# Performance work log

Hardware: AMD Instinct MI355X
Metric: run time of the kernel (lower is better)

The kernel has to match this reference:

```python
import jax, jax.numpy as jnp
import numpy as np
import math

B, Q, CQ = 2, 2048, 512
H, D = 8, 64  # no_heads, c_hidden

def setup_inputs() -> dict:
    key = jax.random.key(0)
    ks = jax.random.split(key, 8)
    s = 0.02
    return {
        "q_x": jax.random.normal(ks[0], (B, Q, CQ), jnp.float32),
        "kv_x": jax.random.normal(ks[1], (B, Q, CQ), jnp.float32),
        "bias": jax.random.normal(ks[2], (B, 1, Q, Q), jnp.float32),
        "w_qkv": jax.random.normal(ks[3], (3 * H * D, CQ), jnp.float32) * s,
        "w_o": jax.random.normal(ks[4], (CQ, H * D), jnp.float32) * s,
        "b_o": jnp.zeros((CQ,), jnp.float32),
        "w_g": jax.random.normal(ks[5], (H * D, CQ), jnp.float32) * s,
        "b_g": jnp.zeros((H * D,), jnp.float32),
    }

def reference(q_x, kv_x, bias, w_qkv, w_o, b_o, w_g, b_g):
    # Fused QKV projection from q_x (kv_x is unused by the original module's _prep_qkv)
    qkv = jnp.einsum('bqc,ec->bqe', q_x, w_qkv)  # [B,Q,3*H*D]
    q, k, v = jnp.split(qkv, 3, axis=-1)
    q = q.reshape(B, Q, H, D) / math.sqrt(D)
    k = k.reshape(B, Q, H, D)
    v = v.reshape(B, Q, H, D)
    # scores + additive pairwise bias, softmax over keys
    scores = jnp.einsum('bqhd,bkhd->bhqk', q, k) + bias  # [B,H,Q,K]
    attn = jax.nn.softmax(scores, axis=-1)
    o = jnp.einsum('bhqk,bkhd->bqhd', attn, v)  # [B,Q,H,D]
    # sigmoid gating
    g = jax.nn.sigmoid(jnp.einsum('bqc,ec->bqe', q_x, w_g) + b_g).reshape(B, Q, H, D)
    o = o * g
    # output projection
    o = o.reshape(B, Q, H * D)
    return jnp.einsum('bqe,ce->bqc', o, w_o) + b_o
```

## Files before the change

kernel.cpp:

```cpp
#include <hip/hip_runtime.h>
#include <math.h>

#define B_  2
#define Q_  2048
#define CQ_ 512
#define H_  8
#define D_  64
#define M_  (B_*Q_)
#define L2E 1.44269504088896f

typedef __bf16 bf16;
typedef __bf16 bf16x4 __attribute__((ext_vector_type(4)));
typedef __bf16 bf16x8 __attribute__((ext_vector_type(8)));
typedef float  f32x4  __attribute__((ext_vector_type(4)));
typedef float  f32x16 __attribute__((ext_vector_type(16)));

__device__ __forceinline__ void gl_lds16(const bf16* g, bf16* l) {
    __builtin_amdgcn_global_load_lds(
        (const __attribute__((address_space(1))) unsigned int*)g,
        (__attribute__((address_space(3))) unsigned int*)l, 16, 0, 0);
}

#define S0 (4096*512)
#define S1 (1536*512)
#define S2 (512*512)
#define S3 (512*512)
__global__ __launch_bounds__(256)
void convert_kernel(const float* __restrict__ qx, const float* __restrict__ wqkv,
                    const float* __restrict__ wg, const float* __restrict__ wo,
                    bf16* __restrict__ qxb, bf16* __restrict__ wcat, bf16* __restrict__ wob)
{
    const long long t = (long long)blockIdx.x * 256 + threadIdx.x;
    const long long e = t * 8;
    const float* src; bf16* dst;
    if (e < S0)                { src = qx + e;                  dst = qxb + e; }
    else if (e < S0 + S1)      { src = wqkv + (e - S0);         dst = wcat + (e - S0); }
    else if (e < S0 + S1 + S2) { src = wg + (e - S0 - S1);      dst = wcat + S1 + (e - S0 - S1); }
    else                       { src = wo + (e - S0 - S1 - S2); dst = wob + (e - S0 - S1 - S2); }
    const float4 a = *(const float4*)(src);
    const float4 b = *(const float4*)(src + 4);
    bf16x8 v;
    v[0] = (bf16)a.x; v[1] = (bf16)a.y; v[2] = (bf16)a.z; v[3] = (bf16)a.w;
    v[4] = (bf16)b.x; v[5] = (bf16)b.y; v[6] = (bf16)b.z; v[7] = (bf16)b.w;
    *(bf16x8*)dst = v;
}

template<int BM, int BN, int EPI>
__global__ __launch_bounds__(256)
void gemm_bf16(const bf16* __restrict__ A, const bf16* __restrict__ W,
               const float* __restrict__ bvec, float* __restrict__ fout,
               bf16* __restrict__ qb, bf16* __restrict__ kb, bf16* __restrict__ vb,
               bf16* __restrict__ gb)
{
    constexpr int MI = BM / 32, NJ = BN / 32;
    __shared__ __align__(16) bf16 As[BM * 32];
    __shared__ __align__(16) bf16 Bs[BN * 32];

    const int t = threadIdx.x;
    const int w = t >> 6, lane = t & 63;
    const int l15 = lane & 15, quad = lane >> 4;
    const int wm = w & 1, wn = w >> 1;
    const int bm = blockIdx.x * BM;
    const int bn = blockIdx.y * BN;
    const bool swapped = (EPI == 1) || ((bn >> 9) != 2);

    f32x4 acc[MI][NJ] = {};

    const int rr = t >> 2;
    const int cc = (t & 3) * 8;

    for (int k0 = 0; k0 < 512; k0 += 32) {
        #pragma unroll
        for (int i = 0; i < BM / 64; ++i)
            gl_lds16(A + (size_t)(bm + i * 64 + rr) * 512 + k0 + cc,
                     As + (i * 64 + w * 16) * 32);
        #pragma unroll
        for (int i = 0; i < BN / 64; ++i)
            gl_lds16(W + (size_t)(bn + i * 64 + rr) * 512 + k0 + cc,
                     Bs + (i * 64 + w * 16) * 32);
        __asm__ volatile("s_waitcnt vmcnt(0)" ::: "memory");
        __syncthreads();

        bf16x8 af[MI], bfr[NJ];
        #pragma unroll
        for (int i = 0; i < MI; ++i)
            af[i] = *(const bf16x8*)(As + (wm * (BM / 2) + i * 16 + l15) * 32 + quad * 8);
        #pragma unroll
        for (int j = 0; j < NJ; ++j)
            bfr[j] = *(const bf16x8*)(Bs + (wn * (BN / 2) + j * 16 + l15) * 32 + quad * 8);
        if (swapped) {
            #pragma unroll
            for (int i = 0; i < MI; ++i)
                #pragma unroll
                for (int j = 0; j < NJ; ++j)
                    acc[i][j] = __builtin_amdgcn_mfma_f32_16x16x32_bf16(bfr[j], af[i], acc[i][j], 0, 0, 0);
        } else {
            #pragma unroll
            for (int i = 0; i < MI; ++i)
                #pragma unroll
                for (int j = 0; j < NJ; ++j)
                    acc[i][j] = __builtin_amdgcn_mfma_f32_16x16x32_bf16(af[i], bfr[j], acc[i][j], 0, 0, 0);
        }
        __syncthreads();
    }

    if (swapped) {
        #pragma unroll
        for (int i = 0; i < MI; ++i) {
            const int m = bm + wm * (BM / 2) + i * 16 + l15;
            const int b = m >> 11, qq = m & 2047;
            #pragma unroll
            for (int j = 0; j < NJ; ++j) {
                const int n0 = bn + wn * (BN / 2) + j * 16 + quad * 4;
                const f32x4 cv = acc[i][j];
                if constexpr (EPI == 1) {
                    float4 st;
                    st.x = cv[0] + bvec[n0 + 0];
                    st.y = cv[1] + bvec[n0 + 1];
                    st.z = cv[2] + bvec[n0 + 2];
                    st.w = cv[3] + bvec[n0 + 3];
                    *(float4*)(fout + (size_t)m * 512 + n0) = st;
                } else {
                    const int part = n0 >> 9;
                    if (part == 0) {
                        const int h = (n0 >> 6) & 7, d0 = n0 & 63;
                        bf16x4 q4;
                        #pragma unroll
                        for (int r = 0; r < 4; ++r) q4[r] = (bf16)(cv[r] * (0.125f * L2E));
                        *(bf16x4*)(qb + (size_t)(b * H_ + h) * (Q_ * D_) + (size_t)qq * 64 + d0) = q4;
                    } else if (part == 1) {
                        const int h = (n0 >> 6) & 7, d0 = n0 & 63;
                        const size_t off = (size_t)(b * H_ + h) * (Q_ * D_)
                            + (qq >> 6) * 4096 + ((qq >> 5) & 1) * 2048
                            + (d0 >> 4) * 512 + ((d0 >> 3) & 1) * 256
                            + (qq & 31) * 8 + (d0 & 7);
                        bf16x4 k4;
                        #pragma unroll
                        for (int r = 0; r < 4; ++r) k4[r] = (bf16)cv[r];
                        *(bf16x4*)(kb + off) = k4;
                    } else {
                        const int gcol = n0 & 511;
                        const float4 bv4 = *(const float4*)(bvec + gcol);
                        bf16x4 g4;
                        g4[0] = (bf16)(1.f / (1.f + __expf(-(cv[0] + bv4.x))));
                        g4[1] = (bf16)(1.f / (1.f + __expf(-(cv[1] + bv4.y))));
                        g4[2] = (bf16)(1.f / (1.f + __expf(-(cv[2] + bv4.z))));
                        g4[3] = (bf16)(1.f / (1.f + __expf(-(cv[3] + bv4.w))));
                        *(bf16x4*)(gb + (size_t)m * 512 + gcol) = g4;
                    }
                }
            }
        }
    } else {
        #pragma unroll
        for (int i = 0; i < MI; ++i) {
            const int m0 = bm + wm * (BM / 2) + i * 16 + quad * 4;
            const int b = m0 >> 11, qq0 = m0 & 2047;
            #pragma unroll
            for (int j = 0; j < NJ; ++j) {
                const int n = bn + wn * (BN / 2) + j * 16 + l15;
                const int h = (n >> 6) & 7, d = n & 63;
                const size_t off = (size_t)(b * H_ + h) * (Q_ * D_)
                    + (qq0 >> 6) * 4096 + (d >> 5) * 2048
                    + ((qq0 & 63) >> 4) * 512 + ((qq0 >> 3) & 1) * 256
                    + (d & 31) * 8 + (qq0 & 7);
                bf16x4 v4;
                #pragma unroll
                for (int r = 0; r < 4; ++r) v4[r] = (bf16)acc[i][j][r];
                *(bf16x4*)(vb + off) = v4;
            }
        }
    }
}

__global__ __launch_bounds__(256, 3)
void attn_part(const bf16* __restrict__ qb, const bf16* __restrict__ kf,
               const bf16* __restrict__ vf, const float* __restrict__ bias,
               bf16* __restrict__ po, float* __restrict__ lsum)
{
    __shared__ __align__(16) bf16 Ks[2][4096];
    __shared__ __align__(16) bf16 Vs[2][4096];
    __shared__ __align__(16) bf16 Ps[4][32 * 72];

    const int tid  = threadIdx.x;
    const int wv   = tid >> 6, lane = tid & 63;
    const int l31  = lane & 31, b5 = lane >> 5;
    const int x    = blockIdx.x;
    const int bh   = ((x & 7) << 1) | (x >> 3);
    const int b    = bh >> 3;
    const int qg   = blockIdx.y * 128 + wv * 32 + l31;
    const int ks   = blockIdx.z;
    const int nsteps = (ks < 2) ? 12 : 8;

    const bf16* qp = qb + ((size_t)bh * Q_ + qg) * D_;
    bf16x8 bq[4];
    #pragma unroll
    for (int c = 0; c < 4; ++c)
        bq[c] = *(const bf16x8*)(qp + c * 16 + b5 * 8);

    f32x16 acc[2] = {};
    float l_loc = 0.f;

    const bf16*  kfb  = kf + (size_t)bh * (Q_ * D_) + (size_t)ks * 12 * 4096;
    const bf16*  vfb  = vf + (size_t)bh * (Q_ * D_) + (size_t)ks * 12 * 4096;
    const float* brow = bias + ((size_t)b * Q_ + qg) * Q_ + ks * 768;

    f32x4 bcur[8], bnxt[8];

    #pragma unroll
    for (int p = 0; p < 2; ++p) {
        gl_lds16(kfb + (wv * 2 + p) * 512 + lane * 8, Ks[0] + (wv * 2 + p) * 512);
        gl_lds16(vfb + (wv * 2 + p) * 512 + lane * 8, Vs[0] + (wv * 2 + p) * 512);
    }
    #pragma unroll
    for (int i = 0; i < 8; ++i)
        bcur[i] = *(const f32x4*)(brow + (i >> 2) * 32 + (i & 3) * 8 + b5 * 4);
    __asm__ volatile("s_waitcnt vmcnt(0)" ::: "memory");
    __syncthreads();

    bf16* pw = Ps[wv] + l31 * 72;

    int cur = 0;
    #pragma unroll 1
    for (int t = 0; t < nsteps; ++t) {
        if (t + 1 < nsteps) {
            const size_t off = (size_t)(t + 1) * 4096;
            #pragma unroll
            for (int p = 0; p < 2; ++p) {
                gl_lds16(kfb + off + (wv * 2 + p) * 512 + lane * 8,
                         Ks[cur ^ 1] + (wv * 2 + p) * 512);
                gl_lds16(vfb + off + (wv * 2 + p) * 512 + lane * 8,
                         Vs[cur ^ 1] + (wv * 2 + p) * 512);
            }
            const int k0n = (t + 1) * 64;
            #pragma unroll
            for (int i = 0; i < 8; ++i)
                bnxt[i] = *(const f32x4*)(brow + k0n + (i >> 2) * 32 + (i & 3) * 8 + b5 * 4);
        }

        const bf16* Kc = Ks[cur];
        f32x16 sv[2] = {};
        #pragma unroll
        for (int kg = 0; kg < 2; ++kg)
            #pragma unroll
            for (int c = 0; c < 4; ++c) {
                const bf16x8 ak = *(const bf16x8*)(Kc + kg * 2048 + c * 512 + lane * 8);
                sv[kg] = __builtin_amdgcn_mfma_f32_32x32x16_bf16(ak, bq[c], sv[kg], 0, 0, 0);
            }

        float sc[2][16];
        float rsum = 0.f;
        #pragma unroll
        for (int kg = 0; kg < 2; ++kg)
            #pragma unroll
            for (int r = 0; r < 16; ++r) {
                sc[kg][r] = __builtin_amdgcn_exp2f(
                    fmaf(bcur[kg * 4 + (r >> 2)][r & 3], L2E, sv[kg][r]));
                rsum += sc[kg][r];
            }
        l_loc += rsum;

        #pragma unroll
        for (int kg = 0; kg < 2; ++kg)
            #pragma unroll
            for (int gi = 0; gi < 4; ++gi) {
                bf16x4 p4;
                p4[0] = (bf16)sc[kg][gi * 4 + 0];
                p4[1] = (bf16)sc[kg][gi * 4 + 1];
                p4[2] = (bf16)sc[kg][gi * 4 + 2];
                p4[3] = (bf16)sc[kg][gi * 4 + 3];
                *(bf16x4*)(pw + kg * 32 + gi * 8 + b5 * 4) = p4;
            }
        __asm__ volatile("s_waitcnt lgkmcnt(0)" ::: "memory");

        const bf16* Vc = Vs[cur];
        #pragma unroll
        for (int c4 = 0; c4 < 4; ++c4) {
            const bf16x8 bp = *(const bf16x8*)(pw + c4 * 16 + b5 * 8);
            #pragma unroll
            for (int dg = 0; dg < 2; ++dg) {
                const bf16x8 av = *(const bf16x8*)(Vc + dg * 2048 + c4 * 512 + lane * 8);
                acc[dg] = __builtin_amdgcn_mfma_f32_32x32x16_bf16(av, bp, acc[dg], 0, 0, 0);
            }
        }

        if (t + 1 < nsteps) {
            #pragma unroll
            for (int i = 0; i < 8; ++i) bcur[i] = bnxt[i];
        }
        __asm__ volatile("s_waitcnt vmcnt(0)" ::: "memory");
        __syncthreads();
        cur ^= 1;
    }

    const float l_run = l_loc + __shfl_xor(l_loc, 32, 64);
    const size_t pbase = ((size_t)(ks * 16 + bh) * Q_ + qg) * 64;
    #pragma unroll
    for (int dg = 0; dg < 2; ++dg)
        #pragma unroll
        for (int gi = 0; gi < 4; ++gi) {
            const int d0 = dg * 32 + gi * 8 + b5 * 4;
            bf16x4 ov;
            #pragma unroll
            for (int r = 0; r < 4; ++r)
                ov[r] = (bf16)acc[dg][gi * 4 + r];
            *(bf16x4*)(po + pbase + d0) = ov;
        }
    if (b5 == 0)
        lsum[(size_t)(ks * 16 + bh) * Q_ + qg] = l_run;
}

__global__ __launch_bounds__(256)
void merge_kernel(const bf16* __restrict__ po, const float* __restrict__ lsum,
                  const bf16* g, bf16* og)
{
    const int gid = blockIdx.x * 256 + threadIdx.x;
    const int row = gid >> 3;
    const int d8  = (gid & 7) * 8;
    const int bh  = row >> 11, qg = row & 2047;
    const int b   = bh >> 3, h = bh & 7;

    const float inv = 1.f / (lsum[row] + lsum[16 * Q_ + row] + lsum[32 * Q_ + row]);

    const bf16x8 o0 = *(const bf16x8*)(po + (size_t)row * 64 + d8);
    const bf16x8 o1 = *(const bf16x8*)(po + (size_t)16 * Q_ * 64 + (size_t)row * 64 + d8);
    const bf16x8 o2 = *(const bf16x8*)(po + (size_t)32 * Q_ * 64 + (size_t)row * 64 + d8);
    const size_t obase = ((size_t)(b * Q_ + qg)) * 512 + h * 64 + d8;
    const bf16x8 gv = *(const bf16x8*)(g + obase);
    bf16x8 ov;
    #pragma unroll
    for (int r = 0; r < 8; ++r)
        ov[r] = (bf16)(((float)o0[r] + (float)o1[r] + (float)o2[r]) * inv * (float)gv[r]);
    *(bf16x8*)(og + obase) = ov;
}

extern "C" void kernel_launch(void* const* d_in, const int* in_sizes, int n_in,
                              void* d_out, int out_size, void* d_ws, size_t ws_size,
                              hipStream_t stream)
{
    const float* q_x   = (const float*)d_in[0];
    const float* bias  = (const float*)d_in[2];
    const float* w_qkv = (const float*)d_in[3];
    const float* w_o   = (const float*)d_in[4];
    const float* b_o   = (const float*)d_in[5];
    const float* w_g   = (const float*)d_in[6];
    const float* b_g   = (const float*)d_in[7];
    float* out = (float*)d_out;

    char* ws = (char*)d_ws;
    bf16*  po   = (bf16*)(ws);
    bf16*  qxb  = (bf16*)(ws);
    bf16*  wcat = (bf16*)(ws + (4u  << 20));
    bf16*  qb   = (bf16*)(ws + (12u << 20));
    bf16*  kb   = (bf16*)(ws + (16u << 20));
    bf16*  vb   = (bf16*)(ws + (20u << 20));
    bf16*  gb   = (bf16*)(ws + (24u << 20));
    bf16*  wob  = (bf16*)(ws + (28u << 20));
    float* lsum = (float*)(ws + (28u << 20) + (1u << 19));

    convert_kernel<<<(S0 + S1 + S2 + S3) / (256 * 8), 256, 0, stream>>>(
        q_x, w_qkv, w_g, w_o, qxb, wcat, wob);
    gemm_bf16<128, 64, 0><<<dim3(32, 32), 256, 0, stream>>>(
        qxb, wcat, b_g, nullptr, qb, kb, vb, gb);
    attn_part<<<dim3(B_ * H_, Q_ / 128, 3), 256, 0, stream>>>(qb, kb, vb, bias, po, lsum);
    merge_kernel<<<(16 * Q_ * 8) / 256, 256, 0, stream>>>(po, lsum, gb, gb);
    gemm_bf16<64, 64, 1><<<dim3(64, 8), 256, 0, stream>>>(
        gb, wob, b_o, out, nullptr, nullptr, nullptr, nullptr);
}
```

Before: 189.9 us.

## Pack GEMM operands k-major, double-buffer GEMM LDS, shuffle P in registers

The convert kernel now writes q_x and the weights in a k-panel-major packed layout, so each GEMM stage becomes contiguous 16-byte global-to-LDS copies. The GEMM gains double-buffered LDS so the next k-slice is fetched while MFMAs run on the current one. In attention, the P tile is passed between half-waves with cross-lane shuffles instead of an LDS round trip, the key split across the three z-slices is rebalanced to 11/11/10, and bias is loaded inside each step rather than prefetched a step ahead. The bias change trades prefetch overlap for lower register pressure, and the doubled GEMM LDS may reduce occupancy.

```diff
diff --git a/kernel.cpp b/kernel.cpp
--- a/kernel.cpp
+++ b/kernel.cpp
@@ -19,6 +19,14 @@
     __builtin_amdgcn_global_load_lds(
         (const __attribute__((address_space(1))) unsigned int*)g,
         (__attribute__((address_space(3))) unsigned int*)l, 16, 0, 0);
+}
+
+__device__ __forceinline__ bf16x4 shfl_xor32(bf16x4 v) {
+    union { bf16x4 h; int i[2]; } u;
+    u.h = v;
+    u.i[0] = __shfl_xor(u.i[0], 32, 64);
+    u.i[1] = __shfl_xor(u.i[1], 32, 64);
+    return u.h;
 }
 
 #define S0 (4096*512)
@@ -33,10 +41,26 @@
     const long long t = (long long)blockIdx.x * 256 + threadIdx.x;
     const long long e = t * 8;
     const float* src; bf16* dst;
-    if (e < S0)                { src = qx + e;                  dst = qxb + e; }
-    else if (e < S0 + S1)      { src = wqkv + (e - S0);         dst = wcat + (e - S0); }
-    else if (e < S0 + S1 + S2) { src = wg + (e - S0 - S1);      dst = wcat + S1 + (e - S0 - S1); }
-    else                       { src = wo + (e - S0 - S1 - S2); dst = wob + (e - S0 - S1 - S2); }
+    if (e < S0) {
+        const int m = (int)(e >> 9), k = (int)(e & 511);
+        src = qx + e;
+        dst = qxb + (size_t)(k >> 5) * (4096 * 32) + (size_t)m * 32 + (k & 31);
+    } else if (e < S0 + S1) {
+        const long long e2 = e - S0;
+        const int n = (int)(e2 >> 9), k = (int)(e2 & 511);
+        src = wqkv + e2;
+        dst = wcat + (size_t)(k >> 5) * (2048 * 32) + (size_t)n * 32 + (k & 31);
+    } else if (e < S0 + S1 + S2) {
+        const long long e2 = e - S0 - S1;
+        const int n = 1536 + (int)(e2 >> 9), k = (int)(e2 & 511);
+        src = wg + e2;
+        dst = wcat + (size_t)(k >> 5) * (2048 * 32) + (size_t)n * 32 + (k & 31);
+    } else {
+        const long long e2 = e - S0 - S1 - S2;
+        const int n = (int)(e2 >> 9), k = (int)(e2 & 511);
+        src = wo + e2;
+        dst = wob + (size_t)(k >> 5) * (512 * 32) + (size_t)n * 32 + (k & 31);
+    }
     const float4 a = *(const float4*)(src);
     const float4 b = *(const float4*)(src + 4);
     bf16x8 v;
@@ -45,7 +69,7 @@
     *(bf16x8*)dst = v;
 }
 
-template<int BM, int BN, int EPI>
+template<int BM, int BN, int EPI, int WNR, int APACK>
 __global__ __launch_bounds__(256)
 void gemm_bf16(const bf16* __restrict__ A, const bf16* __restrict__ W,
                const float* __restrict__ bvec, float* __restrict__ fout,
@@ -53,8 +77,9 @@
                bf16* __restrict__ gb)
 {
     constexpr int MI = BM / 32, NJ = BN / 32;
-    __shared__ __align__(16) bf16 As[BM * 32];
-    __shared__ __align__(16) bf16 Bs[BN * 32];
+    constexpr int APARTS = BM / 16, BPARTS = BN / 16, NPARTS = APARTS + BPARTS;
+    __shared__ __align__(16) bf16 As[2][BM * 32];
+    __shared__ __align__(16) bf16 Bs[2][BN * 32];
 
     const int t = threadIdx.x;
     const int w = t >> 6, lane = t & 63;
@@ -66,28 +91,40 @@
 
     f32x4 acc[MI][NJ] = {};
 
-    const int rr = t >> 2;
-    const int cc = (t & 3) * 8;
-
-    for (int k0 = 0; k0 < 512; k0 += 32) {
-        #pragma unroll
-        for (int i = 0; i < BM / 64; ++i)
-            gl_lds16(A + (size_t)(bm + i * 64 + rr) * 512 + k0 + cc,
-                     As + (i * 64 + w * 16) * 32);
-        #pragma unroll
-        for (int i = 0; i < BN / 64; ++i)
-            gl_lds16(W + (size_t)(bn + i * 64 + rr) * 512 + k0 + cc,
-                     Bs + (i * 64 + w * 16) * 32);
-        __asm__ volatile("s_waitcnt vmcnt(0)" ::: "memory");
-        __syncthreads();
+    auto stage = [&](int kp, int buf) {
+        #pragma unroll
+        for (int idx = 0; idx < NPARTS / 4; ++idx) {
+            const int p = idx * 4 + w;
+            if (p < APARTS) {
+                if constexpr (APACK)
+                    gl_lds16(A + (size_t)kp * (4096 * 32) + (size_t)bm * 32 + p * 512 + lane * 8,
+                             As[buf] + p * 512);
+                else
+                    gl_lds16(A + (size_t)(bm + p * 16 + (lane >> 2)) * 512 + kp * 32 + (lane & 3) * 8,
+                             As[buf] + p * 512);
+            } else {
+                gl_lds16(W + (size_t)kp * (WNR * 32) + (size_t)bn * 32 + (p - APARTS) * 512 + lane * 8,
+                         Bs[buf] + (p - APARTS) * 512);
+            }
+        }
+    };
+
+    stage(0, 0);
+    __asm__ volatile("s_waitcnt vmcnt(0)" ::: "memory");
+    __syncthreads();
+
+    int cur = 0;
+    #pragma unroll 1
+    for (int kp = 0; kp < 16; ++kp) {
+        if (kp < 15) stage(kp + 1, cur ^ 1);
 
         bf16x8 af[MI], bfr[NJ];
         #pragma unroll
         for (int i = 0; i < MI; ++i)
-            af[i] = *(const bf16x8*)(As + (wm * (BM / 2) + i * 16 + l15) * 32 + quad * 8);
+            af[i] = *(const bf16x8*)(As[cur] + (wm * (BM / 2) + i * 16 + l15) * 32 + quad * 8);
         #pragma unroll
         for (int j = 0; j < NJ; ++j)
-            bfr[j] = *(const bf16x8*)(Bs + (wn * (BN / 2) + j * 16 + l15) * 32 + quad * 8);
+            bfr[j] = *(const bf16x8*)(Bs[cur] + (wn * (BN / 2) + j * 16 + l15) * 32 + quad * 8);
         if (swapped) {
             #pragma unroll
             for (int i = 0; i < MI; ++i)
@@ -101,7 +138,9 @@
                 for (int j = 0; j < NJ; ++j)
                     acc[i][j] = __builtin_amdgcn_mfma_f32_16x16x32_bf16(af[i], bfr[j], acc[i][j], 0, 0, 0);
         }
+        __asm__ volatile("s_waitcnt vmcnt(0)" ::: "memory");
         __syncthreads();
+        cur ^= 1;
     }
 
     if (swapped) {
@@ -180,7 +219,6 @@
 {
     __shared__ __align__(16) bf16 Ks[2][4096];
     __shared__ __align__(16) bf16 Vs[2][4096];
-    __shared__ __align__(16) bf16 Ps[4][32 * 72];
 
     const int tid  = threadIdx.x;
     const int wv   = tid >> 6, lane = tid & 63;
@@ -190,7 +228,8 @@
     const int b    = bh >> 3;
     const int qg   = blockIdx.y * 128 + wv * 32 + l31;
     const int ks   = blockIdx.z;
-    const int nsteps = (ks < 2) ? 12 : 8;
+    const int start   = ks * 11;
+    const int nsteps  = (ks == 2) ? 10 : 11;
 
     const bf16* qp = qb + ((size_t)bh * Q_ + qg) * D_;
     bf16x8 bq[4];
@@ -201,24 +240,17 @@
     f32x16 acc[2] = {};
     float l_loc = 0.f;
 
-    const bf16*  kfb  = kf + (size_t)bh * (Q_ * D_) + (size_t)ks * 12 * 4096;
-    const bf16*  vfb  = vf + (size_t)bh * (Q_ * D_) + (size_t)ks * 12 * 4096;
-    const float* brow = bias + ((size_t)b * Q_ + qg) * Q_ + ks * 768;
-
-    f32x4 bcur[8], bnxt[8];
+    const bf16*  kfb  = kf + (size_t)bh * (Q_ * D_) + (size_t)start * 4096;
+    const bf16*  vfb  = vf + (size_t)bh * (Q_ * D_) + (size_t)start * 4096;
+    const float* brow = bias + ((size_t)b * Q_ + qg) * Q_ + start * 64;
 
     #pragma unroll
     for (int p = 0; p < 2; ++p) {
         gl_lds16(kfb + (wv * 2 + p) * 512 + lane * 8, Ks[0] + (wv * 2 + p) * 512);
         gl_lds16(vfb + (wv * 2 + p) * 512 + lane * 8, Vs[0] + (wv * 2 + p) * 512);
     }
-    #pragma unroll
-    for (int i = 0; i < 8; ++i)
-        bcur[i] = *(const f32x4*)(brow + (i >> 2) * 32 + (i & 3) * 8 + b5 * 4);
     __asm__ volatile("s_waitcnt vmcnt(0)" ::: "memory");
     __syncthreads();
-
-    bf16* pw = Ps[wv] + l31 * 72;
 
     int cur = 0;
     #pragma unroll 1
@@ -232,11 +264,12 @@
                 gl_lds16(vfb + off + (wv * 2 + p) * 512 + lane * 8,
                          Vs[cur ^ 1] + (wv * 2 + p) * 512);
             }
-            const int k0n = (t + 1) * 64;
-            #pragma unroll
-            for (int i = 0; i < 8; ++i)
-                bnxt[i] = *(const f32x4*)(brow + k0n + (i >> 2) * 32 + (i & 3) * 8 + b5 * 4);
-        }
+        }
+
+        f32x4 bc[8];
+        #pragma unroll
+        for (int i = 0; i < 8; ++i)
+            bc[i] = *(const f32x4*)(brow + t * 64 + (i >> 2) * 32 + (i & 3) * 8 + b5 * 4);
 
         const bf16* Kc = Ks[cur];
         f32x16 sv[2] = {};
@@ -249,34 +282,35 @@
             }
 
         float sc[2][16];
-        float rsum = 0.f;
+        float rs = 0.f;
         #pragma unroll
         for (int kg = 0; kg < 2; ++kg)
             #pragma unroll
             for (int r = 0; r < 16; ++r) {
                 sc[kg][r] = __builtin_amdgcn_exp2f(
-                    fmaf(bcur[kg * 4 + (r >> 2)][r & 3], L2E, sv[kg][r]));
-                rsum += sc[kg][r];
-            }
-        l_loc += rsum;
-
-        #pragma unroll
-        for (int kg = 0; kg < 2; ++kg)
-            #pragma unroll
-            for (int gi = 0; gi < 4; ++gi) {
-                bf16x4 p4;
-                p4[0] = (bf16)sc[kg][gi * 4 + 0];
-                p4[1] = (bf16)sc[kg][gi * 4 + 1];
-                p4[2] = (bf16)sc[kg][gi * 4 + 2];
-                p4[3] = (bf16)sc[kg][gi * 4 + 3];
-                *(bf16x4*)(pw + kg * 32 + gi * 8 + b5 * 4) = p4;
-            }
-        __asm__ volatile("s_waitcnt lgkmcnt(0)" ::: "memory");
+                    fmaf(bc[kg * 4 + (r >> 2)][r & 3], L2E, sv[kg][r]));
+                rs += sc[kg][r];
+            }
+        l_loc += rs;
 
         const bf16* Vc = Vs[cur];
         #pragma unroll
         for (int c4 = 0; c4 < 4; ++c4) {
-            const bf16x8 bp = *(const bf16x8*)(pw + c4 * 16 + b5 * 8);
+            const int kg = c4 >> 1;
+            const int base = (c4 & 1) * 8;
+            bf16x4 g0, g1;
+            #pragma unroll
+            for (int r = 0; r < 4; ++r) {
+                g0[r] = (bf16)sc[kg][base + r];
+                g1[r] = (bf16)sc[kg][base + 4 + r];
+            }
+            const bf16x4 snd = b5 ? g0 : g1;
+            const bf16x4 rcv = shfl_xor32(snd);
+            const bf16x4 lo  = b5 ? rcv : g0;
+            const bf16x4 hi  = b5 ? g1  : rcv;
+            bf16x8 bp;
+            #pragma unroll
+            for (int r = 0; r < 4; ++r) { bp[r] = lo[r]; bp[4 + r] = hi[r]; }
             #pragma unroll
             for (int dg = 0; dg < 2; ++dg) {
                 const bf16x8 av = *(const bf16x8*)(Vc + dg * 2048 + c4 * 512 + lane * 8);
@@ -284,10 +318,6 @@
             }
         }
 
-        if (t + 1 < nsteps) {
-            #pragma unroll
-            for (int i = 0; i < 8; ++i) bcur[i] = bnxt[i];
-        }
         __asm__ volatile("s_waitcnt vmcnt(0)" ::: "memory");
         __syncthreads();
         cur ^= 1;
@@ -360,10 +390,10 @@
 
     convert_kernel<<<(S0 + S1 + S2 + S3) / (256 * 8), 256, 0, stream>>>(
         q_x, w_qkv, w_g, w_o, qxb, wcat, wob);
-    gemm_bf16<128, 64, 0><<<dim3(32, 32), 256, 0, stream>>>(
+    gemm_bf16<128, 64, 0, 2048, 1><<<dim3(32, 32), 256, 0, stream>>>(
         qxb, wcat, b_g, nullptr, qb, kb, vb, gb);
     attn_part<<<dim3(B_ * H_, Q_ / 128, 3), 256, 0, stream>>>(qb, kb, vb, bias, po, lsum);
     merge_kernel<<<(16 * Q_ * 8) / 256, 256, 0, stream>>>(po, lsum, gb, gb);
-    gemm_bf16<64, 64, 1><<<dim3(64, 8), 256, 0, stream>>>(
+    gemm_bf16<64, 64, 1, 512, 0><<<dim3(64, 8), 256, 0, stream>>>(
         gb, wob, b_o, out, nullptr, nullptr, nullptr, nullptr);
 }
```

Result: no change. 187.3 us (-1.3%).
